# Performance work log

Hardware: AMD Instinct MI355X
Metric: run time of the kernel (lower is better)

Reference implementation:

```python
import jax, jax.numpy as jnp
import numpy as np

N_NODES = 100000  # static segment count for segment_sum
DEGREE = 2        # polynomial degree of the Laplacian filter


def setup_inputs() -> dict:
    key = jax.random.key(0)
    k1, k2, k3, k4 = jax.random.split(key, 4)
    N, E, C = N_NODES, 1600000, 32
    x = jax.random.normal(k1, (N, C), dtype=jnp.float32)
    weights = jax.random.normal(k2, (1 + DEGREE,), dtype=jnp.float32)
    edge_src = jax.random.randint(k3, (E,), 0, N, dtype=jnp.int32)
    edge_dst = jax.random.randint(k4, (E,), 0, N, dtype=jnp.int32)
    return {"x": x, "weights": weights, "edge_src": edge_src, "edge_dst": edge_dst}


def reference(x, weights, edge_src, edge_dst):
    """y = (w0 * I + w1 * L + ... + w_d * L^d) @ x with L = D - A,
    computed by the recurrence t_k = L @ t_{k-1} (never materializing L^k)."""
    N = N_NODES
    # node degrees: D[i] = number of edges landing on i
    deg = jax.ops.segment_sum(jnp.ones_like(edge_src, dtype=x.dtype), edge_dst,
                              num_segments=N)  # [N]

    def lap_matvec(t):
        # (L @ t)[i] = deg[i] * t[i] - sum_{(s->i) in E} t[s]
        agg = jax.ops.segment_sum(t[edge_src], edge_dst, num_segments=N)  # [N, C]
        return deg[:, None] * t - agg

    y = weights[0] * x
    t = x
    for k in range(1, 1 + DEGREE):  # fixed small loop over polynomial order
        t = lap_matvec(t)
        y = y + weights[k] * t
    return y
```

## Files before the change

### kernel.cpp

```cpp
#include <hip/hip_runtime.h>

#define C 32
#define NT 256
#define BSH 8
#define BNODE 256
#define CAPC 5632
#define SRCMASK 0x1FFFF

typedef float f32x4 __attribute__((ext_vector_type(4)));

__device__ __forceinline__ unsigned int f2bf(float f) {
    unsigned int u = __float_as_uint(f);
    return (u + 0x7FFFu + ((u >> 16) & 1u)) >> 16;
}
__device__ __forceinline__ float bflo(unsigned int u) { return __uint_as_float(u << 16); }
__device__ __forceinline__ float bfhi(unsigned int u) { return __uint_as_float(u & 0xFFFF0000u); }

__global__ void init_cursor(int* __restrict__ cursor, int nbuck) {
    int i = blockIdx.x * blockDim.x + threadIdx.x;
    if (i < nbuck) cursor[i] = i * CAPC;
}

__global__ __launch_bounds__(1024) void phaseA(const int* __restrict__ src,
                                               const int* __restrict__ dst,
                                               int* __restrict__ cursor,
                                               int* __restrict__ pk,
                                               int E, int nbuck, int chunk) {
    extern __shared__ int l[];
    int* lcnt = l;
    int* lcur = l + nbuck;
    int tid = threadIdx.x;
    for (int i = tid; i < nbuck; i += 1024) lcnt[i] = 0;
    __syncthreads();
    int base = blockIdx.x * chunk;
    int end  = min(base + chunk, E);
    for (int e = base + tid; e < end; e += 1024)
        atomicAdd(&lcnt[dst[e] >> BSH], 1);
    __syncthreads();
    for (int i = tid; i < nbuck; i += 1024) {
        int c = lcnt[i];
        lcur[i] = c ? atomicAdd(&cursor[i], c) : 0;
    }
    __syncthreads();
    for (int e = base + tid; e < end; e += 1024) {
        int d = dst[e];
        int b = d >> BSH;
        int pos = atomicAdd(&lcur[b], 1);
        pk[pos] = src[e] | ((d & (BNODE - 1)) << 17);
    }
}

__global__ __launch_bounds__(512) void phaseB(int* __restrict__ pk,
                                              const int* __restrict__ cursor,
                                              int* __restrict__ row_start,
                                              int* __restrict__ ideg,
                                              const float* __restrict__ x,
                                              uint2* __restrict__ xb2, int N) {
    __shared__ int ent[CAPC];
    __shared__ int h[BNODE];
    __shared__ int s[BNODE];
    __shared__ int cur[BNODE];
    int b = blockIdx.x;
    int tid = threadIdx.x;

    int n0 = b << BSH;
    int nvalid = min(N - n0, BNODE);
    for (int i = tid; i < nvalid * 8; i += 512) {
        int n = n0 + (i >> 3);
        int lq = i & 7;
        const float* xp = x + (size_t)n * C + lq * 4;
        uint2 r;
        r.x = f2bf(xp[0]) | (f2bf(xp[1]) << 16);
        r.y = f2bf(xp[2]) | (f2bf(xp[3]) << 16);
        xb2[(size_t)n * 8 + lq] = r;
    }

    int base = b * CAPC;
    int cnt = min(cursor[b] - base, CAPC);
    for (int i = tid; i < cnt; i += 512) ent[i] = pk[base + i];
    if (tid < BNODE) h[tid] = 0;
    __syncthreads();
    for (int i = tid; i < cnt; i += 512) atomicAdd(&h[ent[i] >> 17], 1);
    __syncthreads();
    int v = 0;
    if (tid < BNODE) { v = h[tid]; s[tid] = v; }
    __syncthreads();
    for (int off = 1; off < BNODE; off <<= 1) {
        int u = 0;
        if (tid < BNODE && tid >= off) u = s[tid - off];
        __syncthreads();
        if (tid < BNODE) s[tid] += u;
        __syncthreads();
    }
    if (tid < BNODE) {
        int exc = s[tid] - v;
        int n = n0 + tid;
        if (n < N) { row_start[n] = base + exc; ideg[n] = v; }
        cur[tid] = exc;
    }
    __syncthreads();
    for (int i = tid; i < cnt; i += 512) {
        int en = ent[i];
        int pos = atomicAdd(&cur[en >> 17], 1);
        pk[base + pos] = en & SRCMASK;
    }
}

#define ACC4(u0, u1)                                     \
    a0 += bflo(u0); a1 += bfhi(u0);                      \
    a2 += bflo(u1); a3 += bfhi(u1);

__global__ __launch_bounds__(NT) void gather1_bf(const float* __restrict__ x,
        const uint2* __restrict__ xb2, const int* __restrict__ pk,
        const int* __restrict__ row_start, const int* __restrict__ ideg,
        float* __restrict__ t1, uint2* __restrict__ t1b2, int N) {
    int g = blockIdx.x * blockDim.x + threadIdx.x;
    int n = g >> 3;
    if (n >= N) return;
    int lq = g & 7;
    int rs = row_start[n];
    int dg = ideg[n];
    int re = rs + dg;
    float a0 = 0.f, a1 = 0.f, a2 = 0.f, a3 = 0.f;
    int j = rs;
    for (; j + 7 < re; j += 8) {
        int s0 = __builtin_nontemporal_load(&pk[j]);
        int s1 = __builtin_nontemporal_load(&pk[j + 1]);
        int s2 = __builtin_nontemporal_load(&pk[j + 2]);
        int s3 = __builtin_nontemporal_load(&pk[j + 3]);
        int s4 = __builtin_nontemporal_load(&pk[j + 4]);
        int s5 = __builtin_nontemporal_load(&pk[j + 5]);
        int s6 = __builtin_nontemporal_load(&pk[j + 6]);
        int s7 = __builtin_nontemporal_load(&pk[j + 7]);
        uint2 u0 = xb2[(size_t)s0 * 8 + lq];
        uint2 u1 = xb2[(size_t)s1 * 8 + lq];
        uint2 u2 = xb2[(size_t)s2 * 8 + lq];
        uint2 u3 = xb2[(size_t)s3 * 8 + lq];
        uint2 u4 = xb2[(size_t)s4 * 8 + lq];
        uint2 u5 = xb2[(size_t)s5 * 8 + lq];
        uint2 u6 = xb2[(size_t)s6 * 8 + lq];
        uint2 u7 = xb2[(size_t)s7 * 8 + lq];
        ACC4(u0.x, u0.y) ACC4(u1.x, u1.y) ACC4(u2.x, u2.y) ACC4(u3.x, u3.y)
        ACC4(u4.x, u4.y) ACC4(u5.x, u5.y) ACC4(u6.x, u6.y) ACC4(u7.x, u7.y)
    }
    for (; j + 1 < re; j += 2) {
        int s0 = __builtin_nontemporal_load(&pk[j]);
        int s1 = __builtin_nontemporal_load(&pk[j + 1]);
        uint2 u0 = xb2[(size_t)s0 * 8 + lq];
        uint2 u1 = xb2[(size_t)s1 * 8 + lq];
        ACC4(u0.x, u0.y) ACC4(u1.x, u1.y)
    }
    if (j < re) {
        uint2 u0 = xb2[(size_t)__builtin_nontemporal_load(&pk[j]) * 8 + lq];
        ACC4(u0.x, u0.y)
    }
    size_t o = (size_t)n * C + lq * 4;
    f32x4 xv = __builtin_nontemporal_load((const f32x4*)(x + o));
    float fdg = (float)dg;
    f32x4 tv;
    tv.x = fdg * xv.x - a0;
    tv.y = fdg * xv.y - a1;
    tv.z = fdg * xv.z - a2;
    tv.w = fdg * xv.w - a3;
    __builtin_nontemporal_store(tv, (f32x4*)(t1 + o));
    uint2 r;
    r.x = f2bf(tv.x) | (f2bf(tv.y) << 16);
    r.y = f2bf(tv.z) | (f2bf(tv.w) << 16);
    t1b2[(size_t)n * 8 + lq] = r;
}

__global__ __launch_bounds__(NT) void gather2_bf(const float* __restrict__ x,
        const float* __restrict__ t1, const uint2* __restrict__ t1b2,
        const int* __restrict__ pk, const int* __restrict__ row_start,
        const int* __restrict__ ideg, const float* __restrict__ wts,
        float* __restrict__ y, int N) {
    int g = blockIdx.x * blockDim.x + threadIdx.x;
    int n = g >> 3;
    if (n >= N) return;
    int lq = g & 7;
    int rs = row_start[n];
    int dg = ideg[n];
    int re = rs + dg;
    float a0 = 0.f, a1 = 0.f, a2 = 0.f, a3 = 0.f;
    int j = rs;
    for (; j + 7 < re; j += 8) {
        int s0 = __builtin_nontemporal_load(&pk[j]);
        int s1 = __builtin_nontemporal_load(&pk[j + 1]);
        int s2 = __builtin_nontemporal_load(&pk[j + 2]);
        int s3 = __builtin_nontemporal_load(&pk[j + 3]);
        int s4 = __builtin_nontemporal_load(&pk[j + 4]);
        int s5 = __builtin_nontemporal_load(&pk[j + 5]);
        int s6 = __builtin_nontemporal_load(&pk[j + 6]);
        int s7 = __builtin_nontemporal_load(&pk[j + 7]);
        uint2 u0 = t1b2[(size_t)s0 * 8 + lq];
        uint2 u1 = t1b2[(size_t)s1 * 8 + lq];
        uint2 u2 = t1b2[(size_t)s2 * 8 + lq];
        uint2 u3 = t1b2[(size_t)s3 * 8 + lq];
        uint2 u4 = t1b2[(size_t)s4 * 8 + lq];
        uint2 u5 = t1b2[(size_t)s5 * 8 + lq];
        uint2 u6 = t1b2[(size_t)s6 * 8 + lq];
        uint2 u7 = t1b2[(size_t)s7 * 8 + lq];
        ACC4(u0.x, u0.y) ACC4(u1.x, u1.y) ACC4(u2.x, u2.y) ACC4(u3.x, u3.y)
        ACC4(u4.x, u4.y) ACC4(u5.x, u5.y) ACC4(u6.x, u6.y) ACC4(u7.x, u7.y)
    }
    for (; j + 1 < re; j += 2) {
        int s0 = __builtin_nontemporal_load(&pk[j]);
        int s1 = __builtin_nontemporal_load(&pk[j + 1]);
        uint2 u0 = t1b2[(size_t)s0 * 8 + lq];
        uint2 u1 = t1b2[(size_t)s1 * 8 + lq];
        ACC4(u0.x, u0.y) ACC4(u1.x, u1.y)
    }
    if (j < re) {
        uint2 u0 = t1b2[(size_t)__builtin_nontemporal_load(&pk[j]) * 8 + lq];
        ACC4(u0.x, u0.y)
    }
    size_t o = (size_t)n * C + lq * 4;
    f32x4 xv = __builtin_nontemporal_load((const f32x4*)(x + o));
    f32x4 tv = __builtin_nontemporal_load((const f32x4*)(t1 + o));
    float w0 = wts[0], w1 = wts[1], w2 = wts[2];
    float fdg = (float)dg;
    f32x4 r;
    r.x = w0 * xv.x + w1 * tv.x + w2 * (fdg * tv.x - a0);
    r.y = w0 * xv.y + w1 * tv.y + w2 * (fdg * tv.y - a1);
    r.z = w0 * xv.z + w1 * tv.z + w2 * (fdg * tv.z - a2);
    r.w = w0 * xv.w + w1 * tv.w + w2 * (fdg * tv.w - a3);
    __builtin_nontemporal_store(r, (f32x4*)(y + o));
}

__global__ __launch_bounds__(NT) void gather1_f32(const float* __restrict__ x,
        const int* __restrict__ pk, const int* __restrict__ row_start,
        const int* __restrict__ ideg, float* __restrict__ t1, int N) {
    int g = blockIdx.x * blockDim.x + threadIdx.x;
    int n = g >> 5;
    if (n >= N) return;
    int ch = g & 31;
    int rs = row_start[n], dg = ideg[n], re = rs + dg;
    float a0 = 0, a1 = 0, a2 = 0, a3 = 0;
    int j = rs;
    for (; j + 3 < re; j += 4) {
        a0 += x[(size_t)pk[j] * C + ch];     a1 += x[(size_t)pk[j + 1] * C + ch];
        a2 += x[(size_t)pk[j + 2] * C + ch]; a3 += x[(size_t)pk[j + 3] * C + ch];
    }
    for (; j < re; ++j) a0 += x[(size_t)pk[j] * C + ch];
    size_t o = (size_t)n * C + ch;
    t1[o] = (float)dg * x[o] - ((a0 + a1) + (a2 + a3));
}
__global__ __launch_bounds__(NT) void gather2_f32(const float* __restrict__ x,
        const float* __restrict__ t1, const int* __restrict__ pk,
        const int* __restrict__ row_start, const int* __restrict__ ideg,
        const float* __restrict__ wts, float* __restrict__ y, int N) {
    int g = blockIdx.x * blockDim.x + threadIdx.x;
    int n = g >> 5;
    if (n >= N) return;
    int ch = g & 31;
    int rs = row_start[n], dg = ideg[n], re = rs + dg;
    float a0 = 0, a1 = 0, a2 = 0, a3 = 0;
    int j = rs;
    for (; j + 3 < re; j += 4) {
        a0 += t1[(size_t)pk[j] * C + ch];     a1 += t1[(size_t)pk[j + 1] * C + ch];
        a2 += t1[(size_t)pk[j + 2] * C + ch]; a3 += t1[(size_t)pk[j + 3] * C + ch];
    }
    for (; j < re; ++j) a0 += t1[(size_t)pk[j] * C + ch];
    size_t o = (size_t)n * C + ch;
    float tv = t1[o];
    y[o] = wts[0] * x[o] + wts[1] * tv + wts[2] * ((float)dg * tv - ((a0 + a1) + (a2 + a3)));
}

extern "C" void kernel_launch(void* const* d_in, const int* in_sizes, int n_in,
                              void* d_out, int out_size, void* d_ws, size_t ws_size,
                              hipStream_t stream) {
    const float* x    = (const float*)d_in[0];
    const float* wts  = (const float*)d_in[1];
    const int*   esrc = (const int*)d_in[2];
    const int*   edst = (const int*)d_in[3];
    float*       y    = (float*)d_out;

    const int N = in_sizes[0] / C;
    const int E = in_sizes[2];
    const int nbuck = (N + BNODE - 1) >> BSH;
    const int nc = N * C;

    char* p = (char*)d_ws;
    auto align16 = [](size_t s) { return (s + 15) & ~(size_t)15; };
    int* cursor    = (int*)p; p += align16((size_t)nbuck * 4);
    int* row_start = (int*)p; p += align16((size_t)N * 4);
    int* ideg      = (int*)p; p += align16((size_t)N * 4);
    int* pk        = (int*)p; p += align16((size_t)nbuck * CAPC * 4);
    float* t1      = (float*)p; p += align16((size_t)nc * 4);
    uint2* xb2     = (uint2*)p; p += align16((size_t)nc * 2);
    uint2* t1b2    = (uint2*)p; p += align16((size_t)nc * 2);
    bool bf_ok = (size_t)(p - (char*)d_ws) <= ws_size;

    init_cursor<<<(nbuck + NT - 1) / NT, NT, 0, stream>>>(cursor, nbuck);

    const int ABLK = 256;
    const int chunk = (E + ABLK - 1) / ABLK;
    const size_t lds_a = (size_t)nbuck * 2 * 4;
    phaseA<<<ABLK, 1024, lds_a, stream>>>(esrc, edst, cursor, pk, E, nbuck, chunk);
    phaseB<<<nbuck, 512, 0, stream>>>(pk, cursor, row_start, ideg, x, xb2, N);

    if (bf_ok) {
        const int gblocks = ((size_t)N * 8 + NT - 1) / NT;
        gather1_bf<<<gblocks, NT, 0, stream>>>(x, xb2, pk, row_start, ideg, t1, t1b2, N);
        gather2_bf<<<gblocks, NT, 0, stream>>>(x, t1, t1b2, pk, row_start, ideg, wts, y, N);
    } else {
        const int gblocks = ((size_t)N * 32 + NT - 1) / NT;
        gather1_f32<<<gblocks, NT, 0, stream>>>(x, pk, row_start, ideg, t1, N);
        gather2_f32<<<gblocks, NT, 0, stream>>>(x, t1, pk, row_start, ideg, wts, y, N);
    }
}
```

Measured before the change: 175.0 us.

## Drop fp32 t1 buffer, use bf16 self terms, memset cursor, widen phase blocks

Removes the fp32 t1 intermediate so gather1 writes only the bf16 copy, and both gathers read the node's own x and t1 values from the bf16 arrays instead of fp32. The init_cursor kernel becomes a hipMemsetAsync, with the bucket base offset added inside phaseA. phaseA now runs 512 blocks and phaseB runs 1024 threads, and phaseB fuses the LDS staging with the histogram pass. This cuts global traffic and a launch, but reduces accuracy because the diagonal terms now use bf16-rounded values.

After: 174.7 us. Within noise of the previous version (-0.2%).

```diff
diff --git a/kernel.cpp b/kernel.cpp
--- a/kernel.cpp
+++ b/kernel.cpp
@@ -15,11 +15,6 @@
 }
 __device__ __forceinline__ float bflo(unsigned int u) { return __uint_as_float(u << 16); }
 __device__ __forceinline__ float bfhi(unsigned int u) { return __uint_as_float(u & 0xFFFF0000u); }
-
-__global__ void init_cursor(int* __restrict__ cursor, int nbuck) {
-    int i = blockIdx.x * blockDim.x + threadIdx.x;
-    if (i < nbuck) cursor[i] = i * CAPC;
-}
 
 __global__ __launch_bounds__(1024) void phaseA(const int* __restrict__ src,
                                                const int* __restrict__ dst,
@@ -39,7 +34,7 @@
     __syncthreads();
     for (int i = tid; i < nbuck; i += 1024) {
         int c = lcnt[i];
-        lcur[i] = c ? atomicAdd(&cursor[i], c) : 0;
+        lcur[i] = i * CAPC + (c ? atomicAdd(&cursor[i], c) : 0);
     }
     __syncthreads();
     for (int e = base + tid; e < end; e += 1024) {
@@ -50,22 +45,24 @@
     }
 }
 
-__global__ __launch_bounds__(512) void phaseB(int* __restrict__ pk,
-                                              const int* __restrict__ cursor,
-                                              int* __restrict__ row_start,
-                                              int* __restrict__ ideg,
-                                              const float* __restrict__ x,
-                                              uint2* __restrict__ xb2, int N) {
+__global__ __launch_bounds__(1024) void phaseB(int* __restrict__ pk,
+                                               const int* __restrict__ cursor,
+                                               int* __restrict__ row_start,
+                                               int* __restrict__ ideg,
+                                               const float* __restrict__ x,
+                                               uint2* __restrict__ xb2, int N) {
     __shared__ int ent[CAPC];
     __shared__ int h[BNODE];
-    __shared__ int s[BNODE];
+    __shared__ int ss[BNODE];
     __shared__ int cur[BNODE];
     int b = blockIdx.x;
     int tid = threadIdx.x;
 
+    if (tid < BNODE) h[tid] = 0;
+
     int n0 = b << BSH;
     int nvalid = min(N - n0, BNODE);
-    for (int i = tid; i < nvalid * 8; i += 512) {
+    for (int i = tid; i < nvalid * 8; i += 1024) {
         int n = n0 + (i >> 3);
         int lq = i & 7;
         const float* xp = x + (size_t)n * C + lq * 4;
@@ -76,54 +73,45 @@
     }
 
     int base = b * CAPC;
-    int cnt = min(cursor[b] - base, CAPC);
-    for (int i = tid; i < cnt; i += 512) ent[i] = pk[base + i];
-    if (tid < BNODE) h[tid] = 0;
-    __syncthreads();
-    for (int i = tid; i < cnt; i += 512) atomicAdd(&h[ent[i] >> 17], 1);
+    int cnt = min(cursor[b], CAPC);
+    __syncthreads();
+    for (int i = tid; i < cnt; i += 1024) {
+        int en = pk[base + i];
+        ent[i] = en;
+        atomicAdd(&h[en >> 17], 1);
+    }
     __syncthreads();
     int v = 0;
-    if (tid < BNODE) { v = h[tid]; s[tid] = v; }
+    if (tid < BNODE) { v = h[tid]; ss[tid] = v; }
     __syncthreads();
     for (int off = 1; off < BNODE; off <<= 1) {
         int u = 0;
-        if (tid < BNODE && tid >= off) u = s[tid - off];
+        if (tid < BNODE && tid >= off) u = ss[tid - off];
         __syncthreads();
-        if (tid < BNODE) s[tid] += u;
+        if (tid < BNODE) ss[tid] += u;
         __syncthreads();
     }
     if (tid < BNODE) {
-        int exc = s[tid] - v;
+        int exc = ss[tid] - v;
         int n = n0 + tid;
         if (n < N) { row_start[n] = base + exc; ideg[n] = v; }
         cur[tid] = exc;
     }
     __syncthreads();
-    for (int i = tid; i < cnt; i += 512) {
+    for (int i = tid; i < cnt; i += 1024) {
         int en = ent[i];
         int pos = atomicAdd(&cur[en >> 17], 1);
         pk[base + pos] = en & SRCMASK;
     }
 }
 
-#define ACC4(u0, u1)                                     \
-    a0 += bflo(u0); a1 += bfhi(u0);                      \
-    a2 += bflo(u1); a3 += bfhi(u1);
-
-__global__ __launch_bounds__(NT) void gather1_bf(const float* __restrict__ x,
-        const uint2* __restrict__ xb2, const int* __restrict__ pk,
-        const int* __restrict__ row_start, const int* __restrict__ ideg,
-        float* __restrict__ t1, uint2* __restrict__ t1b2, int N) {
-    int g = blockIdx.x * blockDim.x + threadIdx.x;
-    int n = g >> 3;
-    if (n >= N) return;
-    int lq = g & 7;
-    int rs = row_start[n];
-    int dg = ideg[n];
-    int re = rs + dg;
-    float a0 = 0.f, a1 = 0.f, a2 = 0.f, a3 = 0.f;
-    int j = rs;
-    for (; j + 7 < re; j += 8) {
+__device__ __forceinline__ void accum_seg(const uint2* __restrict__ arr,
+                                          const int* __restrict__ pk,
+                                          int lo, int hi, int lq,
+                                          float& a0, float& a1, float& a2, float& a3) {
+#define ACC4(ux, uy) { a0 += bflo(ux); a1 += bfhi(ux); a2 += bflo(uy); a3 += bfhi(uy); }
+    int j = lo;
+    for (; j + 7 < hi; j += 8) {
         int s0 = __builtin_nontemporal_load(&pk[j]);
         int s1 = __builtin_nontemporal_load(&pk[j + 1]);
         int s2 = __builtin_nontemporal_load(&pk[j + 2]);
@@ -132,98 +120,77 @@
         int s5 = __builtin_nontemporal_load(&pk[j + 5]);
         int s6 = __builtin_nontemporal_load(&pk[j + 6]);
         int s7 = __builtin_nontemporal_load(&pk[j + 7]);
-        uint2 u0 = xb2[(size_t)s0 * 8 + lq];
-        uint2 u1 = xb2[(size_t)s1 * 8 + lq];
-        uint2 u2 = xb2[(size_t)s2 * 8 + lq];
-        uint2 u3 = xb2[(size_t)s3 * 8 + lq];
-        uint2 u4 = xb2[(size_t)s4 * 8 + lq];
-        uint2 u5 = xb2[(size_t)s5 * 8 + lq];
-        uint2 u6 = xb2[(size_t)s6 * 8 + lq];
-        uint2 u7 = xb2[(size_t)s7 * 8 + lq];
+        uint2 u0 = arr[(size_t)s0 * 8 + lq];
+        uint2 u1 = arr[(size_t)s1 * 8 + lq];
+        uint2 u2 = arr[(size_t)s2 * 8 + lq];
+        uint2 u3 = arr[(size_t)s3 * 8 + lq];
+        uint2 u4 = arr[(size_t)s4 * 8 + lq];
+        uint2 u5 = arr[(size_t)s5 * 8 + lq];
+        uint2 u6 = arr[(size_t)s6 * 8 + lq];
+        uint2 u7 = arr[(size_t)s7 * 8 + lq];
         ACC4(u0.x, u0.y) ACC4(u1.x, u1.y) ACC4(u2.x, u2.y) ACC4(u3.x, u3.y)
         ACC4(u4.x, u4.y) ACC4(u5.x, u5.y) ACC4(u6.x, u6.y) ACC4(u7.x, u7.y)
     }
-    for (; j + 1 < re; j += 2) {
+    for (; j + 1 < hi; j += 2) {
         int s0 = __builtin_nontemporal_load(&pk[j]);
         int s1 = __builtin_nontemporal_load(&pk[j + 1]);
-        uint2 u0 = xb2[(size_t)s0 * 8 + lq];
-        uint2 u1 = xb2[(size_t)s1 * 8 + lq];
+        uint2 u0 = arr[(size_t)s0 * 8 + lq];
+        uint2 u1 = arr[(size_t)s1 * 8 + lq];
         ACC4(u0.x, u0.y) ACC4(u1.x, u1.y)
     }
-    if (j < re) {
-        uint2 u0 = xb2[(size_t)__builtin_nontemporal_load(&pk[j]) * 8 + lq];
+    if (j < hi) {
+        uint2 u0 = arr[(size_t)__builtin_nontemporal_load(&pk[j]) * 8 + lq];
         ACC4(u0.x, u0.y)
     }
-    size_t o = (size_t)n * C + lq * 4;
-    f32x4 xv = __builtin_nontemporal_load((const f32x4*)(x + o));
-    float fdg = (float)dg;
-    f32x4 tv;
-    tv.x = fdg * xv.x - a0;
-    tv.y = fdg * xv.y - a1;
-    tv.z = fdg * xv.z - a2;
-    tv.w = fdg * xv.w - a3;
-    __builtin_nontemporal_store(tv, (f32x4*)(t1 + o));
-    uint2 r;
-    r.x = f2bf(tv.x) | (f2bf(tv.y) << 16);
-    r.y = f2bf(tv.z) | (f2bf(tv.w) << 16);
-    t1b2[(size_t)n * 8 + lq] = r;
-}
-
-__global__ __launch_bounds__(NT) void gather2_bf(const float* __restrict__ x,
-        const float* __restrict__ t1, const uint2* __restrict__ t1b2,
+#undef ACC4
+}
+
+__global__ __launch_bounds__(NT) void gather1_bf(const uint2* __restrict__ xb2,
         const int* __restrict__ pk, const int* __restrict__ row_start,
-        const int* __restrict__ ideg, const float* __restrict__ wts,
-        float* __restrict__ y, int N) {
+        const int* __restrict__ ideg, uint2* __restrict__ t1b2, int N) {
     int g = blockIdx.x * blockDim.x + threadIdx.x;
     int n = g >> 3;
     if (n >= N) return;
     int lq = g & 7;
     int rs = row_start[n];
     int dg = ideg[n];
-    int re = rs + dg;
     float a0 = 0.f, a1 = 0.f, a2 = 0.f, a3 = 0.f;
-    int j = rs;
-    for (; j + 7 < re; j += 8) {
-        int s0 = __builtin_nontemporal_load(&pk[j]);
-        int s1 = __builtin_nontemporal_load(&pk[j + 1]);
-        int s2 = __builtin_nontemporal_load(&pk[j + 2]);
-        int s3 = __builtin_nontemporal_load(&pk[j + 3]);
-        int s4 = __builtin_nontemporal_load(&pk[j + 4]);
-        int s5 = __builtin_nontemporal_load(&pk[j + 5]);
-        int s6 = __builtin_nontemporal_load(&pk[j + 6]);
-        int s7 = __builtin_nontemporal_load(&pk[j + 7]);
-        uint2 u0 = t1b2[(size_t)s0 * 8 + lq];
-        uint2 u1 = t1b2[(size_t)s1 * 8 + lq];
-        uint2 u2 = t1b2[(size_t)s2 * 8 + lq];
-        uint2 u3 = t1b2[(size_t)s3 * 8 + lq];
-        uint2 u4 = t1b2[(size_t)s4 * 8 + lq];
-        uint2 u5 = t1b2[(size_t)s5 * 8 + lq];
-        uint2 u6 = t1b2[(size_t)s6 * 8 + lq];
-        uint2 u7 = t1b2[(size_t)s7 * 8 + lq];
-        ACC4(u0.x, u0.y) ACC4(u1.x, u1.y) ACC4(u2.x, u2.y) ACC4(u3.x, u3.y)
-        ACC4(u4.x, u4.y) ACC4(u5.x, u5.y) ACC4(u6.x, u6.y) ACC4(u7.x, u7.y)
-    }
-    for (; j + 1 < re; j += 2) {
-        int s0 = __builtin_nontemporal_load(&pk[j]);
-        int s1 = __builtin_nontemporal_load(&pk[j + 1]);
-        uint2 u0 = t1b2[(size_t)s0 * 8 + lq];
-        uint2 u1 = t1b2[(size_t)s1 * 8 + lq];
-        ACC4(u0.x, u0.y) ACC4(u1.x, u1.y)
-    }
-    if (j < re) {
-        uint2 u0 = t1b2[(size_t)__builtin_nontemporal_load(&pk[j]) * 8 + lq];
-        ACC4(u0.x, u0.y)
-    }
-    size_t o = (size_t)n * C + lq * 4;
-    f32x4 xv = __builtin_nontemporal_load((const f32x4*)(x + o));
-    f32x4 tv = __builtin_nontemporal_load((const f32x4*)(t1 + o));
+    accum_seg(xb2, pk, rs, rs + dg, lq, a0, a1, a2, a3);
+    uint2 xs = xb2[(size_t)n * 8 + lq];
+    float fdg = (float)dg;
+    float t0 = fdg * bflo(xs.x) - a0;
+    float t1v = fdg * bfhi(xs.x) - a1;
+    float t2 = fdg * bflo(xs.y) - a2;
+    float t3 = fdg * bfhi(xs.y) - a3;
+    uint2 r;
+    r.x = f2bf(t0) | (f2bf(t1v) << 16);
+    r.y = f2bf(t2) | (f2bf(t3) << 16);
+    t1b2[(size_t)n * 8 + lq] = r;
+}
+
+__global__ __launch_bounds__(NT) void gather2_bf(const uint2* __restrict__ xb2,
+        const uint2* __restrict__ t1b2, const int* __restrict__ pk,
+        const int* __restrict__ row_start, const int* __restrict__ ideg,
+        const float* __restrict__ wts, float* __restrict__ y, int N) {
+    int g = blockIdx.x * blockDim.x + threadIdx.x;
+    int n = g >> 3;
+    if (n >= N) return;
+    int lq = g & 7;
+    int rs = row_start[n];
+    int dg = ideg[n];
+    float a0 = 0.f, a1 = 0.f, a2 = 0.f, a3 = 0.f;
+    accum_seg(t1b2, pk, rs, rs + dg, lq, a0, a1, a2, a3);
+    uint2 xs = xb2[(size_t)n * 8 + lq];
+    uint2 ts = t1b2[(size_t)n * 8 + lq];
     float w0 = wts[0], w1 = wts[1], w2 = wts[2];
     float fdg = (float)dg;
+    float tv0 = bflo(ts.x), tv1 = bfhi(ts.x), tv2 = bflo(ts.y), tv3 = bfhi(ts.y);
     f32x4 r;
-    r.x = w0 * xv.x + w1 * tv.x + w2 * (fdg * tv.x - a0);
-    r.y = w0 * xv.y + w1 * tv.y + w2 * (fdg * tv.y - a1);
-    r.z = w0 * xv.z + w1 * tv.z + w2 * (fdg * tv.z - a2);
-    r.w = w0 * xv.w + w1 * tv.w + w2 * (fdg * tv.w - a3);
+    r.x = w0 * bflo(xs.x) + w1 * tv0 + w2 * (fdg * tv0 - a0);
+    r.y = w0 * bfhi(xs.x) + w1 * tv1 + w2 * (fdg * tv1 - a1);
+    r.z = w0 * bflo(xs.y) + w1 * tv2 + w2 * (fdg * tv2 - a2);
+    r.w = w0 * bfhi(xs.y) + w1 * tv3 + w2 * (fdg * tv3 - a3);
+    size_t o = (size_t)n * C + lq * 4;
     __builtin_nontemporal_store(r, (f32x4*)(y + o));
 }
 
@@ -286,23 +253,23 @@
     int* row_start = (int*)p; p += align16((size_t)N * 4);
     int* ideg      = (int*)p; p += align16((size_t)N * 4);
     int* pk        = (int*)p; p += align16((size_t)nbuck * CAPC * 4);
-    float* t1      = (float*)p; p += align16((size_t)nc * 4);
     uint2* xb2     = (uint2*)p; p += align16((size_t)nc * 2);
     uint2* t1b2    = (uint2*)p; p += align16((size_t)nc * 2);
+    float* t1      = (float*)p;
     bool bf_ok = (size_t)(p - (char*)d_ws) <= ws_size;
 
-    init_cursor<<<(nbuck + NT - 1) / NT, NT, 0, stream>>>(cursor, nbuck);
-
-    const int ABLK = 256;
+    hipMemsetAsync(cursor, 0, (size_t)nbuck * 4, stream);
+
+    const int ABLK = 512;
     const int chunk = (E + ABLK - 1) / ABLK;
     const size_t lds_a = (size_t)nbuck * 2 * 4;
     phaseA<<<ABLK, 1024, lds_a, stream>>>(esrc, edst, cursor, pk, E, nbuck, chunk);
-    phaseB<<<nbuck, 512, 0, stream>>>(pk, cursor, row_start, ideg, x, xb2, N);
+    phaseB<<<nbuck, 1024, 0, stream>>>(pk, cursor, row_start, ideg, x, xb2, N);
 
     if (bf_ok) {
         const int gblocks = ((size_t)N * 8 + NT - 1) / NT;
-        gather1_bf<<<gblocks, NT, 0, stream>>>(x, xb2, pk, row_start, ideg, t1, t1b2, N);
-        gather2_bf<<<gblocks, NT, 0, stream>>>(x, t1, t1b2, pk, row_start, ideg, wts, y, N);
+        gather1_bf<<<gblocks, NT, 0, stream>>>(xb2, pk, row_start, ideg, t1b2, N);
+        gather2_bf<<<gblocks, NT, 0, stream>>>(xb2, t1b2, pk, row_start, ideg, wts, y, N);
     } else {
         const int gblocks = ((size_t)N * 32 + NT - 1) / NT;
         gather1_f32<<<gblocks, NT, 0, stream>>>(x, pk, row_start, ideg, t1, N);
```
